# Kernel optimization log

Measured on AMD Instinct MI355X. Metric: run time of the kernel, lower is better.

The kernel has to match this reference:

```python
import jax, jax.numpy as jnp
import numpy as np
import math

H = 4
D_MODEL = 512
OUT_DIM = D_MODEL // 2  # 256 (concat=True path)
D_K = OUT_DIM // H      # 64
N = 4096


def setup_inputs() -> dict:
    key0 = jax.random.key(0)
    ks = jax.random.split(key0, 12)
    s = 1.0 / math.sqrt(D_MODEL)
    inp = {
        "query": jax.random.normal(ks[0], (N, D_MODEL), dtype=jnp.float32),
        "key": jax.random.normal(ks[1], (N, D_MODEL), dtype=jnp.float32),
        "mask": jax.random.randint(ks[2], (N, N), 0, 2, dtype=jnp.int32),
        # 4 linears (q, k, q_v, k_v), each d_model -> out_dim
        "Wq": jax.random.normal(ks[3], (OUT_DIM, D_MODEL), dtype=jnp.float32) * s,
        "bq": jax.random.normal(ks[4], (OUT_DIM,), dtype=jnp.float32) * s,
        "Wk": jax.random.normal(ks[5], (OUT_DIM, D_MODEL), dtype=jnp.float32) * s,
        "bk": jax.random.normal(ks[6], (OUT_DIM,), dtype=jnp.float32) * s,
        "Wqv": jax.random.normal(ks[7], (OUT_DIM, D_MODEL), dtype=jnp.float32) * s,
        "bqv": jax.random.normal(ks[8], (OUT_DIM,), dtype=jnp.float32) * s,
        "Wkv": jax.random.normal(ks[9], (OUT_DIM, D_MODEL), dtype=jnp.float32) * s,
        "bkv": jax.random.normal(ks[10], (OUT_DIM,), dtype=jnp.float32) * s,
    }
    return inp


def _heads(x, W, b):
    # [N, d_model] @ W^T + b -> [N, out_dim] -> [h, N, d_k]
    y = x @ W.T + b
    return y.reshape(-1, H, D_K).transpose(1, 0, 2)


def reference(query, key, mask, Wq, bq, Wk, bk, Wqv, bqv, Wkv, bkv):
    q = _heads(query, Wq, bq)    # [h, Nq, d_k]
    k = _heads(key, Wk, bk)      # [h, Nk, d_k]
    qv = _heads(query, Wqv, bqv)  # [h, Nq, d_k]
    kv = _heads(key, Wkv, bkv)    # [h, Nk, d_k]

    scores = jnp.einsum("hqd,hkd->hqk", q, k) / math.sqrt(D_K)  # [h, Nq, Nk]
    scores = jnp.where(mask[None] == 0, jnp.float32(-1e9), scores)
    p = jax.nn.softmax(scores, axis=-1)  # attention weights per head

    # x1 = ELU(p @ k_v), x2 = ELU(p^T @ q_v); concat over heads.
    x1 = jax.nn.elu(jnp.einsum("hqk,hkd->hqd", p, kv))  # [h, Nq, d_k]
    x2 = jax.nn.elu(jnp.einsum("hqk,hqd->hkd", p, qv))  # [h, Nk, d_k]
    x1 = x1.transpose(1, 0, 2).reshape(-1, H * D_K)  # [Nq, out_dim]
    x2 = x2.transpose(1, 0, 2).reshape(-1, H * D_K)  # [Nk, out_dim]
    # Dropout omitted (inference / deterministic reference).
    return x1, x2, p
```

## Files before the change

### kernel.cpp

```cpp
#include <hip/hip_runtime.h>
#include <hip/hip_bf16.h>

#define NN 4096
#define DMODEL 512
#define ODIM 256
#define NHEAD 4
#define DKH 64
#define NKW 64

typedef __attribute__((ext_vector_type(8))) short short8;
typedef __attribute__((ext_vector_type(4))) short short4v;
typedef __attribute__((ext_vector_type(8))) __bf16 bf16x8;
typedef __attribute__((ext_vector_type(4))) float f32x4;

__device__ __forceinline__ short f2bf(float f) {
    unsigned u = __builtin_bit_cast(unsigned, f);
    u += 0x7fffu + ((u >> 16) & 1u);
    return (short)(u >> 16);
}
__device__ __forceinline__ float bf2f(short s) {
    unsigned u = ((unsigned)(unsigned short)s) << 16;
    return __builtin_bit_cast(float, u);
}
__device__ __forceinline__ f32x4 mfma16(short8 a, short8 b, f32x4 c) {
    return __builtin_amdgcn_mfma_f32_16x16x32_bf16(
        __builtin_bit_cast(bf16x8, a), __builtin_bit_cast(bf16x8, b), c, 0, 0, 0);
}

__global__ __launch_bounds__(256) void pack_mask_k(const int* __restrict__ mask,
                                                   unsigned long long* __restrict__ bits) {
    int tid = blockIdx.x * 256 + threadIdx.x;
    int wid = tid >> 6;
    int lane = tid & 63;
    int v = __builtin_nontemporal_load(mask + (size_t)wid * 64 + lane);
    unsigned long long b = __ballot(v != 0);
    if (lane == 0) bits[wid] = b;
}

__global__ __launch_bounds__(256) void proj_k(
    const float* __restrict__ Xq, const float* __restrict__ Xk,
    const float* __restrict__ Wq, const float* __restrict__ bq,
    const float* __restrict__ Wk, const float* __restrict__ bk,
    const float* __restrict__ Wqv, const float* __restrict__ bqv,
    const float* __restrict__ Wkv, const float* __restrict__ bkv,
    short* __restrict__ qh, short* __restrict__ kh,
    short* __restrict__ qvT, short* __restrict__ kvT) {
    int z = blockIdx.z;
    const float *X, *W, *B;
    short* out;
    int tr;
    float postscale = 1.f;
    switch (z) {
        case 0: X = Xq; W = Wq;  B = bq;  out = qh;  tr = 0; postscale = 0.125f; break;
        case 1: X = Xk; W = Wk;  B = bk;  out = kh;  tr = 0; break;
        case 2: X = Xq; W = Wqv; B = bqv; out = qvT; tr = 1; break;
        default: X = Xk; W = Wkv; B = bkv; out = kvT; tr = 1; break;
    }
    int lane = threadIdx.x & 63, w = threadIdx.x >> 6;
    int lr = lane & 15, lg = lane >> 4;
    int m0 = blockIdx.x * 64 + (w >> 1) * 32;
    int n0 = blockIdx.y * 64 + (w & 1) * 32;

    f32x4 acc[2][2] = {};
    for (int kk = 0; kk < DMODEL; kk += 32) {
        short8 a[2], b[2];
#pragma unroll
        for (int i = 0; i < 2; i++) {
            const float* pa = X + (size_t)(m0 + i * 16 + lr) * DMODEL + kk + lg * 8;
            const float* pb = W + (size_t)(n0 + i * 16 + lr) * DMODEL + kk + lg * 8;
            float4 a0 = *(const float4*)pa;
            float4 a1 = *(const float4*)(pa + 4);
            float4 b0 = *(const float4*)pb;
            float4 b1 = *(const float4*)(pb + 4);
            a[i][0] = f2bf(a0.x); a[i][1] = f2bf(a0.y); a[i][2] = f2bf(a0.z); a[i][3] = f2bf(a0.w);
            a[i][4] = f2bf(a1.x); a[i][5] = f2bf(a1.y); a[i][6] = f2bf(a1.z); a[i][7] = f2bf(a1.w);
            b[i][0] = f2bf(b0.x); b[i][1] = f2bf(b0.y); b[i][2] = f2bf(b0.z); b[i][3] = f2bf(b0.w);
            b[i][4] = f2bf(b1.x); b[i][5] = f2bf(b1.y); b[i][6] = f2bf(b1.z); b[i][7] = f2bf(b1.w);
        }
#pragma unroll
        for (int i = 0; i < 2; i++)
#pragma unroll
            for (int j = 0; j < 2; j++) acc[i][j] = mfma16(a[i], b[j], acc[i][j]);
    }
#pragma unroll
    for (int i = 0; i < 2; i++)
#pragma unroll
        for (int j = 0; j < 2; j++) {
            int col = n0 + j * 16 + lr;
            float bv = B[col];
            int hh = col >> 6, dk = col & 63;
#pragma unroll
            for (int r = 0; r < 4; r++) {
                int row = m0 + i * 16 + lg * 4 + r;
                short s = f2bf((acc[i][j][r] + bv) * postscale);
                if (!tr) out[((size_t)hh * NN + row) * DKH + dk] = s;
                else     out[((size_t)hh * DKH + dk) * NN + row] = s;
            }
        }
}

__global__ __launch_bounds__(512) void attn_fused_k(
    const short* __restrict__ qh, const short* __restrict__ kh, const short* __restrict__ kvT,
    const unsigned long long* __restrict__ bits,
    short* __restrict__ pbuf, float* __restrict__ linv_ws,
    float* __restrict__ x1_out, float* __restrict__ p_out) {
    int h = blockIdx.y;
    int strip = blockIdx.x;
    int tid = threadIdx.x, lane = tid & 63, w = tid >> 6;
    int lr = lane & 15, lg = lane >> 4;
    int q0 = strip * 16;

    __shared__ float smemf[4608];
    short (*plds)[16][72] = (short (*)[16][72])smemf;
    float (*xbuf)[64][17] = (float (*)[64][17])smemf;
    __shared__ float sl[8][16];
    __shared__ float linv_s[16];

    const short* khh = kh + (size_t)h * NN * DKH;
    const unsigned long long* brow = bits + (size_t)(q0 + lr) * NKW;
    short* ptile0 = pbuf + (((size_t)(h * 256 + strip) * 64) << 10);

    short8 bq[2];
#pragma unroll
    for (int kk = 0; kk < 2; kk++)
        bq[kk] = *(const short8*)(qh + ((size_t)h * NN + q0 + lr) * DKH + kk * 32 + lg * 8);

    float lrun = 0.f;
    f32x4 acc1[4] = {};
    for (int t = 0; t < 8; t++) {
        int kt = w * 8 + t;
        f32x4 s[4] = {};
#pragma unroll
        for (int fj = 0; fj < 4; fj++)
#pragma unroll
            for (int kk = 0; kk < 2; kk++) {
                short8 a = *(const short8*)(khh + (size_t)(kt * 64 + fj * 16 + lr) * DKH + kk * 32 + lg * 8);
                s[fj] = mfma16(a, bq[kk], s[fj]);
            }
        unsigned long long mw = brow[kt] >> (lg * 4);
        short* ptile = ptile0 + ((size_t)kt << 10);
#pragma unroll
        for (int fj = 0; fj < 4; fj++) {
            short4v pb4;
#pragma unroll
            for (int r = 0; r < 4; r++) {
                bool keep = (mw >> (fj * 16 + r)) & 1ull;
                float e = __expf(keep ? s[fj][r] : -100.f);
                lrun += e;
                pb4[r] = f2bf(e);
            }
            *(short4v*)&plds[w][lr][fj * 16 + lg * 4] = pb4;
#pragma unroll
            for (int r = 0; r < 4; r++)
                ptile[(fj * 16 + lg * 4 + r) * 16 + lr] = pb4[r];
        }
#pragma unroll
        for (int kk = 0; kk < 2; kk++) {
            short8 a1 = *(const short8*)&plds[w][lr][kk * 32 + lg * 8];
#pragma unroll
            for (int fd = 0; fd < 4; fd++) {
                short8 bv = *(const short8*)(kvT + ((size_t)h * DKH + fd * 16 + lr) * NN + kt * 64 + kk * 32 + lg * 8);
                acc1[fd] = mfma16(a1, bv, acc1[fd]);
            }
        }
    }
    lrun += __shfl_xor(lrun, 16);
    lrun += __shfl_xor(lrun, 32);
    if (lg == 0) sl[w][lr] = lrun;
    __syncthreads();
    float l = 0.f;
#pragma unroll
    for (int w2 = 0; w2 < 8; w2++) l += sl[w2][lr];
    float linv = l > 0.f ? 1.f / l : 0.f;
    if (w == 0 && lg == 0) {
        linv_s[lr] = linv;
        linv_ws[(size_t)h * NN + q0 + lr] = linv;
    }
    __syncthreads();

    asm volatile("s_waitcnt vmcnt(0)" ::: "memory");
    float linvv[16];
#pragma unroll
    for (int j = 0; j < 16; j++) linvv[j] = linv_s[j];
    for (int t = 0; t < 8; t++) {
        int kt = w * 8 + t;
        const short* tl = ptile0 + ((size_t)kt << 10) + lane * 16;
        float* pd = p_out + ((size_t)h * NN + q0) * NN + kt * 64 + lane;
#pragma unroll
        for (int qh2 = 0; qh2 < 2; qh2++) {
            short8 pv = *(const short8*)(tl + qh2 * 8);
#pragma unroll
            for (int j = 0; j < 8; j++) {
                int q = qh2 * 8 + j;
                pd[(size_t)q * NN] = bf2f(pv[j]) * linvv[q];
            }
        }
    }

    __syncthreads();
    if (w >= 4) {
#pragma unroll
        for (int fd = 0; fd < 4; fd++)
#pragma unroll
            for (int r = 0; r < 4; r++) xbuf[w - 4][lane][fd * 4 + r] = acc1[fd][r];
    }
    __syncthreads();
    if (w < 4) {
#pragma unroll
        for (int fd = 0; fd < 4; fd++)
#pragma unroll
            for (int r = 0; r < 4; r++) acc1[fd][r] += xbuf[w][lane][fd * 4 + r];
    }
    __syncthreads();
    if (w >= 1 && w < 4) {
#pragma unroll
        for (int fd = 0; fd < 4; fd++)
#pragma unroll
            for (int r = 0; r < 4; r++) xbuf[w - 1][lane][fd * 4 + r] = acc1[fd][r];
    }
    __syncthreads();
    if (w == 0) {
#pragma unroll
        for (int fd = 0; fd < 4; fd++)
#pragma unroll
            for (int r = 0; r < 4; r++) {
                float v = acc1[fd][r] + xbuf[0][lane][fd * 4 + r] + xbuf[1][lane][fd * 4 + r] +
                          xbuf[2][lane][fd * 4 + r];
                v *= linv_s[lg * 4 + r];
                v = v > 0.f ? v : (__expf(v) - 1.f);
                x1_out[(size_t)(q0 + lg * 4 + r) * ODIM + h * DKH + fd * 16 + lr] = v;
            }
    }
}

__global__ __launch_bounds__(256) void scale_qv_k(const short* __restrict__ qvT,
                                                  const float* __restrict__ linv,
                                                  short* __restrict__ qvS) {
    int idx = blockIdx.x * 256 + threadIdx.x;
    int q8 = idx & 511;
    int dh = idx >> 9;
    int h = dh >> 6;
    short8 v = *(const short8*)(qvT + (size_t)dh * NN + q8 * 8);
    const float* lp = linv + (size_t)h * NN + q8 * 8;
    float4 l0 = *(const float4*)lp;
    float4 l1 = *(const float4*)(lp + 4);
    short8 o;
    o[0] = f2bf(bf2f(v[0]) * l0.x); o[1] = f2bf(bf2f(v[1]) * l0.y);
    o[2] = f2bf(bf2f(v[2]) * l0.z); o[3] = f2bf(bf2f(v[3]) * l0.w);
    o[4] = f2bf(bf2f(v[4]) * l1.x); o[5] = f2bf(bf2f(v[5]) * l1.y);
    o[6] = f2bf(bf2f(v[6]) * l1.z); o[7] = f2bf(bf2f(v[7]) * l1.w);
    *(short8*)(qvS + (size_t)dh * NN + q8 * 8) = o;
}

__global__ __launch_bounds__(512) void px2b_k(
    const short* __restrict__ pbuf, const short* __restrict__ qvS,
    float* __restrict__ x2part) {
    int kt = blockIdx.x, h = blockIdx.y, z = blockIdx.z;
    int tid = threadIdx.x, lane = tid & 63, w = tid >> 6;
    int fj = w & 3, sh = w >> 2;
    int lr = lane & 15, lg = lane >> 4;

    __shared__ float red[4][64][17];

    const short* qvh = qvS + (size_t)h * DKH * NN;
    f32x4 acc[4] = {};
    int qbase = z * 1024 + sh * 512;

#pragma unroll 4
    for (int it = 0; it < 16; it++) {
        int qq = qbase + it * 32;
        int strip = (qq >> 4) + (lg >> 1);
        const short* ap = pbuf + (((size_t)(h * 256 + strip) * 64 + kt) << 10) +
                          (fj * 16 + lr) * 16 + (lg & 1) * 8;
        short8 af = *(const short8*)ap;
#pragma unroll
        for (int fd = 0; fd < 4; fd++) {
            short8 bv = *(const short8*)(qvh + (size_t)(fd * 16 + lr) * NN + qq + lg * 8);
            acc[fd] = mfma16(af, bv, acc[fd]);
        }
    }
    if (sh == 1) {
#pragma unroll
        for (int fd = 0; fd < 4; fd++)
#pragma unroll
            for (int r = 0; r < 4; r++) red[fj][lane][fd * 4 + r] = acc[fd][r];
    }
    __syncthreads();
    if (sh == 0) {
        float* xp = x2part + (size_t)z * NN * ODIM;
#pragma unroll
        for (int fd = 0; fd < 4; fd++)
#pragma unroll
            for (int r = 0; r < 4; r++) {
                float v = acc[fd][r] + red[fj][lane][fd * 4 + r];
                xp[(size_t)(kt * 64 + fj * 16 + lg * 4 + r) * ODIM + h * DKH + fd * 16 + lr] = v;
            }
    }
}

__global__ __launch_bounds__(256) void combine_x2_k(const float* __restrict__ x2part,
                                                    float* __restrict__ x2_out) {
    int idx = blockIdx.x * 256 + threadIdx.x;
    size_t i = (size_t)idx * 4;
    const size_t stride = (size_t)NN * ODIM;
    float4 a = *(const float4*)(x2part + i);
    float4 b = *(const float4*)(x2part + stride + i);
    float4 c = *(const float4*)(x2part + 2 * stride + i);
    float4 d = *(const float4*)(x2part + 3 * stride + i);
    float4 o;
    o.x = a.x + b.x + c.x + d.x;
    o.y = a.y + b.y + c.y + d.y;
    o.z = a.z + b.z + c.z + d.z;
    o.w = a.w + b.w + c.w + d.w;
    o.x = o.x > 0.f ? o.x : (__expf(o.x) - 1.f);
    o.y = o.y > 0.f ? o.y : (__expf(o.y) - 1.f);
    o.z = o.z > 0.f ? o.z : (__expf(o.z) - 1.f);
    o.w = o.w > 0.f ? o.w : (__expf(o.w) - 1.f);
    *(float4*)(x2_out + i) = o;
}

__global__ __launch_bounds__(512) void attn_fb_k(
    const short* __restrict__ qh, const short* __restrict__ kh, const short* __restrict__ kvT,
    const unsigned long long* __restrict__ bits,
    float* __restrict__ x1_out, float* __restrict__ p_out) {
    int h = blockIdx.y;
    int tid = threadIdx.x, lane = tid & 63, w = tid >> 6;
    int lr = lane & 15, lg = lane >> 4;
    int q0 = blockIdx.x * 16;

    __shared__ float smemf[4608];
    short (*plds)[16][72] = (short (*)[16][72])smemf;
    float (*xbuf)[64][17] = (float (*)[64][17])smemf;
    __shared__ float sl[8][16];

    const short* khh = kh + (size_t)h * NN * DKH;
    const unsigned long long* brow = bits + (size_t)(q0 + lr) * NKW;

    short8 bq[2];
#pragma unroll
    for (int kk = 0; kk < 2; kk++)
        bq[kk] = *(const short8*)(qh + ((size_t)h * NN + q0 + lr) * DKH + kk * 32 + lg * 8);

    float lrun = 0.f;
    for (int t = 0; t < 8; t++) {
        int kt = w * 8 + t;
        f32x4 s[4] = {};
#pragma unroll
        for (int fj = 0; fj < 4; fj++)
#pragma unroll
            for (int kk = 0; kk < 2; kk++) {
                short8 a = *(const short8*)(khh + (size_t)(kt * 64 + fj * 16 + lr) * DKH + kk * 32 + lg * 8);
                s[fj] = mfma16(a, bq[kk], s[fj]);
            }
        unsigned long long mw = brow[kt] >> (lg * 4);
#pragma unroll
        for (int fj = 0; fj < 4; fj++)
#pragma unroll
            for (int r = 0; r < 4; r++) {
                bool keep = (mw >> (fj * 16 + r)) & 1ull;
                lrun += __expf(keep ? s[fj][r] : -100.f);
            }
    }
    lrun += __shfl_xor(lrun, 16);
    lrun += __shfl_xor(lrun, 32);
    if (lg == 0) sl[w][lr] = lrun;
    __syncthreads();
    float l = 0.f;
#pragma unroll
    for (int w2 = 0; w2 < 8; w2++) l += sl[w2][lr];
    float linv = l > 0.f ? 1.f / l : 0.f;

    f32x4 acc1[4] = {};
    float* prow = p_out + ((size_t)h * NN + q0 + lr) * NN;
    for (int t = 0; t < 8; t++) {
        int kt = w * 8 + t;
        f32x4 s[4] = {};
#pragma unroll
        for (int fj = 0; fj < 4; fj++)
#pragma unroll
            for (int kk = 0; kk < 2; kk++) {
                short8 a = *(const short8*)(khh + (size_t)(kt * 64 + fj * 16 + lr) * DKH + kk * 32 + lg * 8);
                s[fj] = mfma16(a, bq[kk], s[fj]);
            }
        unsigned long long mw = brow[kt] >> (lg * 4);
#pragma unroll
        for (int fj = 0; fj < 4; fj++) {
            float4 pv;
            short4v pb;
#pragma unroll
            for (int r = 0; r < 4; r++) {
                bool keep = (mw >> (fj * 16 + r)) & 1ull;
                float p = __expf(keep ? s[fj][r] : -100.f) * linv;
                (&pv.x)[r] = p;
                pb[r] = f2bf(p);
            }
            *(float4*)(prow + kt * 64 + fj * 16 + lg * 4) = pv;
            *(short4v*)&plds[w][lr][fj * 16 + lg * 4] = pb;
        }
#pragma unroll
        for (int kk = 0; kk < 2; kk++) {
            short8 a1 = *(const short8*)&plds[w][lr][kk * 32 + lg * 8];
#pragma unroll
            for (int fd = 0; fd < 4; fd++) {
                short8 bv = *(const short8*)(kvT + ((size_t)h * DKH + fd * 16 + lr) * NN + kt * 64 + kk * 32 + lg * 8);
                acc1[fd] = mfma16(a1, bv, acc1[fd]);
            }
        }
    }
    __syncthreads();
    if (w >= 4) {
#pragma unroll
        for (int fd = 0; fd < 4; fd++)
#pragma unroll
            for (int r = 0; r < 4; r++) xbuf[w - 4][lane][fd * 4 + r] = acc1[fd][r];
    }
    __syncthreads();
    if (w < 4) {
#pragma unroll
        for (int fd = 0; fd < 4; fd++)
#pragma unroll
            for (int r = 0; r < 4; r++) acc1[fd][r] += xbuf[w][lane][fd * 4 + r];
    }
    __syncthreads();
    if (w >= 1 && w < 4) {
#pragma unroll
        for (int fd = 0; fd < 4; fd++)
#pragma unroll
            for (int r = 0; r < 4; r++) xbuf[w - 1][lane][fd * 4 + r] = acc1[fd][r];
    }
    __syncthreads();
    if (w == 0) {
#pragma unroll
        for (int fd = 0; fd < 4; fd++)
#pragma unroll
            for (int r = 0; r < 4; r++) {
                float v = acc1[fd][r] + xbuf[0][lane][fd * 4 + r] + xbuf[1][lane][fd * 4 + r] +
                          xbuf[2][lane][fd * 4 + r];
                v = v > 0.f ? v : (__expf(v) - 1.f);
                x1_out[(size_t)(q0 + lg * 4 + r) * ODIM + h * DKH + fd * 16 + lr] = v;
            }
    }
}

__global__ __launch_bounds__(512) void px2_fb_k(
    const float* __restrict__ p, const short* __restrict__ qvT,
    float* __restrict__ x2_out) {
    int h = blockIdx.y;
    int k0 = blockIdx.x * 32;
    int tid = threadIdx.x, lane = tid & 63, w = tid >> 6;
    int lr = lane & 15, lg = lane >> 4;

    __shared__ float red[4][64][33];

    f32x4 acc[2][4] = {};
    const float* pbase = p + (size_t)h * NN * NN;
    const short* qvh = qvT + (size_t)h * DKH * NN;

    for (int it = 0; it < 16; it++) {
        int qq = w * 512 + it * 32;
        short8 aP[2];
#pragma unroll
        for (int fj = 0; fj < 2; fj++) {
            const float* pp = pbase + (size_t)(qq + lg * 8) * NN + k0 + fj * 16 + lr;
            short8 av;
#pragma unroll
            for (int j = 0; j < 8; j++) av[j] = f2bf(pp[j * NN]);
            aP[fj] = av;
        }
#pragma unroll
        for (int fd = 0; fd < 4; fd++) {
            short8 bv = *(const short8*)(qvh + (size_t)(fd * 16 + lr) * NN + qq + lg * 8);
#pragma unroll
            for (int fj = 0; fj < 2; fj++) acc[fj][fd] = mfma16(aP[fj], bv, acc[fj][fd]);
        }
    }
    if (w >= 4) {
#pragma unroll
        for (int fj = 0; fj < 2; fj++)
#pragma unroll
            for (int fd = 0; fd < 4; fd++)
#pragma unroll
                for (int r = 0; r < 4; r++)
                    red[w - 4][lane][fj * 16 + fd * 4 + r] = acc[fj][fd][r];
    }
    __syncthreads();
    if (w < 4) {
#pragma unroll
        for (int fj = 0; fj < 2; fj++)
#pragma unroll
            for (int fd = 0; fd < 4; fd++)
#pragma unroll
                for (int r = 0; r < 4; r++)
                    acc[fj][fd][r] += red[w][lane][fj * 16 + fd * 4 + r];
    }
    __syncthreads();
    if (w >= 1 && w < 4) {
#pragma unroll
        for (int fj = 0; fj < 2; fj++)
#pragma unroll
            for (int fd = 0; fd < 4; fd++)
#pragma unroll
                for (int r = 0; r < 4; r++)
                    red[w - 1][lane][fj * 16 + fd * 4 + r] = acc[fj][fd][r];
    }
    __syncthreads();
    if (w == 0) {
#pragma unroll
        for (int fj = 0; fj < 2; fj++)
#pragma unroll
            for (int fd = 0; fd < 4; fd++)
#pragma unroll
                for (int r = 0; r < 4; r++) {
                    float v = acc[fj][fd][r];
#pragma unroll
                    for (int s2 = 0; s2 < 3; s2++) v += red[s2][lane][fj * 16 + fd * 4 + r];
                    v = v > 0.f ? v : (__expf(v) - 1.f);
                    x2_out[(size_t)(k0 + fj * 16 + lg * 4 + r) * ODIM + h * DKH + fd * 16 + lr] = v;
                }
    }
}

extern "C" void kernel_launch(void* const* d_in, const int* in_sizes, int n_in,
                              void* d_out, int out_size, void* d_ws, size_t ws_size,
                              hipStream_t stream) {
    (void)in_sizes; (void)n_in; (void)out_size;
    const float* query = (const float*)d_in[0];
    const float* key   = (const float*)d_in[1];
    const int*   mask  = (const int*)d_in[2];
    const float* Wq  = (const float*)d_in[3];
    const float* bq  = (const float*)d_in[4];
    const float* Wk  = (const float*)d_in[5];
    const float* bk  = (const float*)d_in[6];
    const float* Wqv = (const float*)d_in[7];
    const float* bqv = (const float*)d_in[8];
    const float* Wkv = (const float*)d_in[9];
    const float* bkv = (const float*)d_in[10];

    float* out = (float*)d_out;
    float* x1 = out;
    float* x2 = out + (size_t)NN * ODIM;
    float* p  = out + (size_t)2 * NN * ODIM;

    char* ws = (char*)d_ws;
    short* qh  = (short*)(ws);
    short* kh  = (short*)(ws + (2ull << 20));
    short* qvT = (short*)(ws + (4ull << 20));
    short* kvT = (short*)(ws + (6ull << 20));
    unsigned long long* bits = (unsigned long long*)(ws + (8ull << 20));
    float* linv_ws = (float*)(ws + (10ull << 20));
    short* qvS = (short*)(ws + (10ull << 20) + (1ull << 19));
    float* x2part = (float*)(ws + (13ull << 20));
    short* pbuf = (short*)(ws + (29ull << 20));
    size_t need = (29ull << 20) + (size_t)NHEAD * NN * NN * sizeof(short);

    hipLaunchKernelGGL(pack_mask_k, dim3(NN * NN / 64 / 4), dim3(256), 0, stream, mask, bits);
    hipLaunchKernelGGL(proj_k, dim3(64, 4, 4), dim3(256), 0, stream,
                       query, key, Wq, bq, Wk, bk, Wqv, bqv, Wkv, bkv, qh, kh, qvT, kvT);

    if (ws_size >= need) {
        hipLaunchKernelGGL(attn_fused_k, dim3(NN / 16, NHEAD), dim3(512), 0, stream,
                           qh, kh, kvT, bits, pbuf, linv_ws, x1, p);
        hipLaunchKernelGGL(scale_qv_k, dim3(512), dim3(256), 0, stream, qvT, linv_ws, qvS);
        hipLaunchKernelGGL(px2b_k, dim3(NN / 64, NHEAD, 4), dim3(512), 0, stream,
                           pbuf, qvS, x2part);
        hipLaunchKernelGGL(combine_x2_k, dim3(NN * ODIM / 4 / 256), dim3(256), 0, stream,
                           x2part, x2);
    } else {
        hipLaunchKernelGGL(attn_fb_k, dim3(NN / 16, NHEAD), dim3(512), 0, stream,
                           qh, kh, kvT, bits, x1, p);
        hipLaunchKernelGGL(px2_fb_k, dim3(NN / 32, NHEAD), dim3(512), 0, stream,
                           p, qvT, x2);
    }
}
```

Baseline: 359.8 us.

## Vectorize P tile stores via LDS transpose and software-prefetch loads in P writeout and x2 GEMM

The per-element scattered 2-byte stores of the bf16 P tile are replaced by reading the tile back transposed from shared memory and writing two 16-byte vectors per lane. The final P normalization/writeout loop and the px2b x2 GEMM loop now prefetch the next iteration's tiles into registers, a double-buffering scheme meant to hide global load latency. This costs extra LDS reads, more register pressure, and possibly lower occupancy.

```diff
diff --git a/kernel.cpp b/kernel.cpp
--- a/kernel.cpp
+++ b/kernel.cpp
@@ -138,7 +138,6 @@
                 s[fj] = mfma16(a, bq[kk], s[fj]);
             }
         unsigned long long mw = brow[kt] >> (lg * 4);
-        short* ptile = ptile0 + ((size_t)kt << 10);
 #pragma unroll
         for (int fj = 0; fj < 4; fj++) {
             short4v pb4;
@@ -150,9 +149,6 @@
                 pb4[r] = f2bf(e);
             }
             *(short4v*)&plds[w][lr][fj * 16 + lg * 4] = pb4;
-#pragma unroll
-            for (int r = 0; r < 4; r++)
-                ptile[(fj * 16 + lg * 4 + r) * 16 + lr] = pb4[r];
         }
 #pragma unroll
         for (int kk = 0; kk < 2; kk++) {
@@ -162,6 +158,16 @@
                 short8 bv = *(const short8*)(kvT + ((size_t)h * DKH + fd * 16 + lr) * NN + kt * 64 + kk * 32 + lg * 8);
                 acc1[fd] = mfma16(a1, bv, acc1[fd]);
             }
+        }
+        {
+            short8 v0, v1;
+#pragma unroll
+            for (int j = 0; j < 8; j++) v0[j] = plds[w][j][lane];
+#pragma unroll
+            for (int j = 0; j < 8; j++) v1[j] = plds[w][8 + j][lane];
+            short* ptile = ptile0 + ((size_t)kt << 10) + lane * 16;
+            *(short8*)(ptile) = v0;
+            *(short8*)(ptile + 8) = v1;
         }
     }
     lrun += __shfl_xor(lrun, 16);
@@ -182,19 +188,23 @@
     float linvv[16];
 #pragma unroll
     for (int j = 0; j < 16; j++) linvv[j] = linv_s[j];
+    const short* tl0 = ptile0 + ((size_t)(w * 8) << 10) + lane * 16;
+    short8 pv0 = *(const short8*)(tl0);
+    short8 pv1 = *(const short8*)(tl0 + 8);
     for (int t = 0; t < 8; t++) {
         int kt = w * 8 + t;
-        const short* tl = ptile0 + ((size_t)kt << 10) + lane * 16;
+        short8 n0 = pv0, n1 = pv1;
+        if (t < 7) {
+            const short* tn = ptile0 + ((size_t)(kt + 1) << 10) + lane * 16;
+            n0 = *(const short8*)(tn);
+            n1 = *(const short8*)(tn + 8);
+        }
         float* pd = p_out + ((size_t)h * NN + q0) * NN + kt * 64 + lane;
 #pragma unroll
-        for (int qh2 = 0; qh2 < 2; qh2++) {
-            short8 pv = *(const short8*)(tl + qh2 * 8);
-#pragma unroll
-            for (int j = 0; j < 8; j++) {
-                int q = qh2 * 8 + j;
-                pd[(size_t)q * NN] = bf2f(pv[j]) * linvv[q];
-            }
-        }
+        for (int j = 0; j < 8; j++) pd[(size_t)j * NN] = bf2f(pv0[j]) * linvv[j];
+#pragma unroll
+        for (int j = 0; j < 8; j++) pd[(size_t)(8 + j) * NN] = bf2f(pv1[j]) * linvv[8 + j];
+        pv0 = n0; pv1 = n1;
     }
 
     __syncthreads();
@@ -266,18 +276,32 @@
     f32x4 acc[4] = {};
     int qbase = z * 1024 + sh * 512;
 
-#pragma unroll 4
+    int qq0 = qbase;
+    int strip0 = (qq0 >> 4) + (lg >> 1);
+    short8 afc = *(const short8*)(pbuf + (((size_t)(h * 256 + strip0) * 64 + kt) << 10) +
+                                  (fj * 16 + lr) * 16 + (lg & 1) * 8);
+    short8 bvc0 = *(const short8*)(qvh + (size_t)(0 * 16 + lr) * NN + qq0 + lg * 8);
+    short8 bvc1 = *(const short8*)(qvh + (size_t)(1 * 16 + lr) * NN + qq0 + lg * 8);
+    short8 bvc2 = *(const short8*)(qvh + (size_t)(2 * 16 + lr) * NN + qq0 + lg * 8);
+    short8 bvc3 = *(const short8*)(qvh + (size_t)(3 * 16 + lr) * NN + qq0 + lg * 8);
+
     for (int it = 0; it < 16; it++) {
-        int qq = qbase + it * 32;
-        int strip = (qq >> 4) + (lg >> 1);
-        const short* ap = pbuf + (((size_t)(h * 256 + strip) * 64 + kt) << 10) +
-                          (fj * 16 + lr) * 16 + (lg & 1) * 8;
-        short8 af = *(const short8*)ap;
-#pragma unroll
-        for (int fd = 0; fd < 4; fd++) {
-            short8 bv = *(const short8*)(qvh + (size_t)(fd * 16 + lr) * NN + qq + lg * 8);
-            acc[fd] = mfma16(af, bv, acc[fd]);
-        }
+        short8 afn = afc, bvn0 = bvc0, bvn1 = bvc1, bvn2 = bvc2, bvn3 = bvc3;
+        if (it < 15) {
+            int qq = qbase + (it + 1) * 32;
+            int strip = (qq >> 4) + (lg >> 1);
+            afn = *(const short8*)(pbuf + (((size_t)(h * 256 + strip) * 64 + kt) << 10) +
+                                   (fj * 16 + lr) * 16 + (lg & 1) * 8);
+            bvn0 = *(const short8*)(qvh + (size_t)(0 * 16 + lr) * NN + qq + lg * 8);
+            bvn1 = *(const short8*)(qvh + (size_t)(1 * 16 + lr) * NN + qq + lg * 8);
+            bvn2 = *(const short8*)(qvh + (size_t)(2 * 16 + lr) * NN + qq + lg * 8);
+            bvn3 = *(const short8*)(qvh + (size_t)(3 * 16 + lr) * NN + qq + lg * 8);
+        }
+        acc[0] = mfma16(afc, bvc0, acc[0]);
+        acc[1] = mfma16(afc, bvc1, acc[1]);
+        acc[2] = mfma16(afc, bvc2, acc[2]);
+        acc[3] = mfma16(afc, bvc3, acc[3]);
+        afc = afn; bvc0 = bvn0; bvc1 = bvn1; bvc2 = bvn2; bvc3 = bvn3;
     }
     if (sh == 1) {
 #pragma unroll
```

Result: faster. 344.9 us (-4.1%).
